# Kernel tuning notes

Measured on AMD Instinct MI355X. Metric: run time of the kernel, lower is better.

Reference implementation:

```python
import jax, jax.numpy as jnp
import numpy as np

B, P, D = 256, 128, 768        # batch, property slots per sample, encoder hidden dim
E = 64                          # num_properties (number of adapter heads)
H = 256                         # adapter_hidden_dim
H2 = H // 2
O = 2                           # output_dim
LN_EPS = 1e-5
RES_W_ADPT, RES_W_BASE = 0.7, 0.3


def setup_inputs() -> dict:
    key = jax.random.key(0)
    ks = jax.random.split(key, 12)
    hidden_states = jax.random.normal(ks[0], (B, P, D), dtype=jnp.float32)
    base_output = jax.random.normal(ks[1], (B, P, O), dtype=jnp.float32)
    properties = jax.random.randint(ks[2], (B, P), 0, E, dtype=jnp.int64)
    mask = (jax.random.uniform(ks[3], (B, P)) > 0.1).astype(jnp.float32)
    # Stacked per-head adapter parameters (LayerNorm + 3 Linears per head)
    ln_g = jnp.ones((E, D), dtype=jnp.float32)
    ln_b = jnp.zeros((E, D), dtype=jnp.float32)
    W1 = jax.random.normal(ks[4], (E, D, H), dtype=jnp.float32) * (1.0 / np.sqrt(D))
    b1 = jnp.zeros((E, H), dtype=jnp.float32)
    W2 = jax.random.normal(ks[5], (E, H, H2), dtype=jnp.float32) * (1.0 / np.sqrt(H))
    b2 = jnp.zeros((E, H2), dtype=jnp.float32)
    W3 = jax.random.normal(ks[6], (E, H2, O), dtype=jnp.float32) * 0.01  # init std=0.01 per source
    b3 = jnp.zeros((E, O), dtype=jnp.float32)
    return {
        "hidden_states": hidden_states, "base_output": base_output,
        "properties": properties, "mask": mask,
        "ln_g": ln_g, "ln_b": ln_b, "W1": W1, "b1": b1,
        "W2": W2, "b2": b2, "W3": W3, "b3": b3,
    }


def reference(hidden_states, base_output, properties, mask,
              ln_g, ln_b, W1, b1, W2, b2, W3, b3):
    b, p, d = hidden_states.shape
    o = W3.shape[-1]
    x = hidden_states.reshape(-1, d)                        # [N, D]
    # LayerNorm statistics are head-independent; only gamma/beta differ per head
    mu = jnp.mean(x, axis=-1, keepdims=True)
    var = jnp.mean((x - mu) ** 2, axis=-1, keepdims=True)
    xhat = (x - mu) * jax.lax.rsqrt(var + LN_EPS)           # [N, D]
    flat_p = properties.reshape(-1)                         # [N]
    flat_m = mask.reshape(-1)                               # [N]

    def body(acc, inp):
        idx, g, bt, w1, bb1, w2, bb2, w3, bb3 = inp
        h = jax.nn.relu((xhat * g + bt) @ w1 + bb1)         # [N, H]  (dropout = identity in eval)
        h = jax.nn.relu(h @ w2 + bb2)                       # [N, H2]
        out = h @ w3 + bb3                                  # [N, O]
        sel = (flat_p == idx) & (flat_m > 0)
        return jnp.where(sel[:, None], out, acc), None

    e = W1.shape[0]
    acc0 = jnp.zeros((b * p, o), dtype=x.dtype)
    acc, _ = jax.lax.scan(
        body, acc0,
        (jnp.arange(e), ln_g, ln_b, W1, b1, W2, b2, W3, b3))
    out = acc.reshape(b, p, o)
    out = RES_W_ADPT * out + RES_W_BASE * base_output       # use_residual=True
    return out * mask[..., None]
```

## Files before the change

kernel.cpp:

```cpp
#include <hip/hip_runtime.h>
#include <stdint.h>

typedef unsigned short u16;
typedef unsigned int   u32;

#define NTOK   32768
#define GD     768
#define GH     256
#define GH2    128
#define GE     64

typedef __bf16 bf16x8 __attribute__((ext_vector_type(8)));
typedef float  f32x4  __attribute__((ext_vector_type(4)));
union Frag { uint4 u; bf16x8 b; };

__device__ __forceinline__ float bf2f(u16 h) {
  union { u32 u; float f; } v; v.u = ((u32)h) << 16; return v.f;
}
__device__ __forceinline__ u16 f2bf(float f) {
  union { float f; u32 u; } v; v.f = f;
  u32 r = (v.u + 0x7fffu + ((v.u >> 16) & 1u)) >> 16;
  return (u16)r;
}

__device__ __forceinline__ void async16(void* lds, const void* g) {
  __builtin_amdgcn_global_load_lds(
      (const __attribute__((address_space(1))) void*)g,
      (__attribute__((address_space(3))) void*)lds, 16, 0, 0);
}

__device__ __forceinline__ int getProp(const int* p32, int t, int is64) {
  return is64 ? p32[2 * t] : p32[t];
}

static const size_t OFF_W1T  = 0;
static const size_t OFF_W2T  = 25165824;
static const size_t OFF_TOK  = 29360128;
static const size_t OFF_META = 29491200;

__global__ void setup_kernel(const int* __restrict__ prop, const float* __restrict__ mask,
                             u32* __restrict__ outz, int* __restrict__ counts2d,
                             int* __restrict__ cursors_p, int* __restrict__ flagp) {
  __shared__ int h[GE];
  __shared__ int vOr;
  const int b = blockIdx.x;
  const int tid = threadIdx.x;
  outz[b * 512 + tid] = 0u;
  outz[b * 512 + 256 + tid] = 0u;
  if (b < 4) cursors_p[b * 256 + tid] = 0;
  if (tid < GE) h[tid] = 0;
  if (tid == 0) vOr = 0;
  __syncthreads();
  int v = prop[2 * tid + 1] | prop[2 * (tid + 256) + 1];
  if (v) atomicOr(&vOr, 1);
  __syncthreads();
  const int is64 = (vOr == 0) ? 1 : 0;
  if (b == 0 && tid == 0) *flagp = is64;
  const int t = b * 256 + tid;
  if (mask[t] > 0.f) atomicAdd(&h[getProp(prop, t, is64)], 1);
  __syncthreads();
  if (tid < GE) counts2d[b * GE + tid] = h[tid];
}

__global__ void transpose_w1(const float* __restrict__ in, u16* __restrict__ out) {
  __shared__ u16 tl[64][260];
  const int bid = blockIdx.x;
  const int e  = bid / 12, r = bid % 12;
  const int d0 = (r / 4) * 256, h0 = (r % 4) * 64;
  const int tid = threadIdx.x;
  const size_t inMat = (size_t)e * GD * GH;
  const size_t outMat = (size_t)e * GH * GD;
  const int h_l = (tid & 15) * 4, d_l = tid >> 4;
#pragma unroll
  for (int dd = 0; dd < 16; ++dd) {
    const int d = d_l + dd * 16;
    float4 v = *(const float4*)(in + inMat + (size_t)(d0 + d) * GH + h0 + h_l);
    tl[h_l + 0][d] = f2bf(v.x);
    tl[h_l + 1][d] = f2bf(v.y);
    tl[h_l + 2][d] = f2bf(v.z);
    tl[h_l + 3][d] = f2bf(v.w);
  }
  __syncthreads();
  const int wv = tid >> 6, ln = tid & 63;
#pragma unroll
  for (int hh = 0; hh < 16; ++hh) {
    const int h = wv * 16 + hh;
    *(uint2*)(out + outMat + (size_t)(h0 + h) * GD + d0 + ln * 4) =
        *(const uint2*)&tl[h][ln * 4];
  }
}

__global__ void transpose_kernel(const float* __restrict__ in, u16* __restrict__ out,
                                 int R, int C, int tilesC) {
  __shared__ u16 tile[32][33];
  const int tilesPerMat = (R >> 5) * tilesC;
  const int e  = blockIdx.x / tilesPerMat;
  const int t  = blockIdx.x % tilesPerMat;
  const int tr = t / tilesC, tc = t % tilesC;
  const size_t mat = (size_t)e * R * C;
  const int tx = threadIdx.x & 31, ty = threadIdx.x >> 5;
  const int r0 = tr * 32, c0 = tc * 32;
#pragma unroll
  for (int i = 0; i < 32; i += 8)
    tile[ty + i][tx] = f2bf(in[mat + (size_t)(r0 + ty + i) * C + c0 + tx]);
  __syncthreads();
#pragma unroll
  for (int i = 0; i < 32; i += 8)
    out[mat + (size_t)(c0 + ty + i) * R + r0 + tx] = tile[tx][ty + i];
}

__global__ void scan_kernel(const int* __restrict__ counts2d, int* __restrict__ offsets,
                            int* __restrict__ tileHead, int* __restrict__ tileRow,
                            int* __restrict__ nTilesPtr) {
  __shared__ int part[4][GE];
  const int tid = threadIdx.x;
  const int e = tid & 63, q = tid >> 6;
  int c = 0;
  for (int b = q * 32; b < q * 32 + 32; ++b) c += counts2d[b * GE + e];
  part[q][e] = c;
  __syncthreads();
  if (tid < GE) {
    const int ct = part[0][e] + part[1][e] + part[2][e] + part[3][e];
    int inc = ct;
#pragma unroll
    for (int d = 1; d < 64; d <<= 1) { int n = __shfl_up(inc, d); if (e >= d) inc += n; }
    const int off = inc - ct;
    offsets[e] = off;
    if (e == 63) offsets[64] = inc;
    int ntile = (ct + 63) >> 6;
    int inct = ntile;
#pragma unroll
    for (int d = 1; d < 64; d <<= 1) { int n = __shfl_up(inct, d); if (e >= d) inct += n; }
    const int tb = inct - ntile;
    for (int j = 0; j < ntile; ++j) { tileHead[tb + j] = e; tileRow[tb + j] = off + j * 64; }
    if (e == 63) *nTilesPtr = inct;
  }
}

__global__ void scatter_kernel(const int* __restrict__ prop, const float* __restrict__ mask,
                               const int* __restrict__ offsets, int* __restrict__ cursors_p,
                               int* __restrict__ tokenIds, const int* __restrict__ flag) {
  __shared__ int h[GE];
  __shared__ int basebin[GE];
  const int tid = threadIdx.x;
  const int t = blockIdx.x * 256 + tid;
  if (tid < GE) h[tid] = 0;
  __syncthreads();
  int p = -1, rank = 0;
  if (mask[t] > 0.f) {
    p = getProp(prop, t, *flag);
    rank = atomicAdd(&h[p], 1);
  }
  __syncthreads();
  if (tid < GE && h[tid] > 0) basebin[tid] = atomicAdd(&cursors_p[tid * 16], h[tid]);
  __syncthreads();
  if (p >= 0) tokenIds[offsets[p] + basebin[p] + rank] = t;
}

__global__ __launch_bounds__(256, 2) void adapter_gemm(
    const float* __restrict__ hs, const u16* __restrict__ w1t, const u16* __restrict__ w2t,
    const float* __restrict__ lng, const float* __restrict__ lnb,
    const float* __restrict__ b1, const float* __restrict__ b2,
    const float* __restrict__ w3, const float* __restrict__ b3,
    const float* __restrict__ base, const float* __restrict__ mask,
    const int* __restrict__ tokenIds, const int* __restrict__ offsets,
    const int* __restrict__ tileHead, const int* __restrict__ tileRow,
    const int* __restrict__ nTilesPtr, float* __restrict__ outp) {
  __shared__ union LU {
    struct { u16 A[2][2048]; u16 B[2][8192]; } s;
    u16 h[17408];
  } uni;
  __shared__ u16 sB2[2][4096];
  __shared__ float sBias1[256];
  __shared__ float sBias2[128];
  __shared__ float sW3[2][128];
  __shared__ float sB3[2];
  __shared__ int   sTok[64];
  __shared__ __align__(16) float sGam[GD];
  __shared__ __align__(16) float sBet[GD];
  __shared__ float sMu[64];
  __shared__ float sRstd[64];

  const int tid  = threadIdx.x;
  const int wv   = tid >> 6;
  const int ln   = tid & 63;
  const int l15  = tid & 15;
  const int quad = (tid & 63) >> 4;
  const f32x4 vzero = {0.f, 0.f, 0.f, 0.f};
  const int nt = *nTilesPtr;

  for (int tile = blockIdx.x; tile < nt; tile += gridDim.x) {
    __syncthreads();
    const int e  = tileHead[tile];
    const int rs = tileRow[tile];
    const int nRows = min(64, offsets[e + 1] - rs);

    if (tid < 64) sTok[tid] = tokenIds[rs + min(tid, nRows - 1)];
    sBias1[tid] = b1[e * GH + tid];
    if (tid < 128) sBias2[tid] = b2[e * GH2 + tid];
    { const int k = tid >> 1, o = tid & 1; sW3[o][k] = w3[e * GH2 * 2 + k * 2 + o]; }
    if (tid < 2) sB3[tid] = b3[e * 2 + tid];
    __syncthreads();

    const u16* w1e = w1t + (size_t)e * GH * GD;
    const u16* w2e = w2t + (size_t)e * GH2 * GH;

#pragma unroll
    for (int j = 0; j < 4; ++j)
      async16(uni.s.B[0] + wv * 2048 + j * 512,
              w1e + (size_t)(j * 64 + ln) * GD + wv * 8);

    if (tid < 192) {
      *(float4*)&sGam[tid * 4] = *(const float4*)(lng + (size_t)e * GD + tid * 4);
      *(float4*)&sBet[tid * 4] = *(const float4*)(lnb + (size_t)e * GD + tid * 4);
    }

#pragma unroll 2
    for (int pass = 0; pass < 4; ++pass) {
      const int row = pass * 16 + (tid >> 4);
      const int l16 = tid & 15;
      const float* xp = hs + (size_t)sTok[row] * GD + l16 * 4;
      float s = 0.f, sq = 0.f;
#pragma unroll
      for (int c = 0; c < 12; ++c) {
        float4 u = *(const float4*)(xp + c * 64);
        s  += u.x + u.y + u.z + u.w;
        sq += u.x*u.x + u.y*u.y + u.z*u.z + u.w*u.w;
      }
#pragma unroll
      for (int d = 1; d < 16; d <<= 1) { s += __shfl_xor(s, d); sq += __shfl_xor(sq, d); }
      if (l16 == 0) {
        const float mu = s * (1.f / 768.f);
        sMu[row] = mu;
        sRstd[row] = rsqrtf(sq * (1.f / 768.f) - mu * mu + 1e-5f);
      }
    }
    __syncthreads();

    const int r0  = tid >> 3;
    const int klo = (tid & 7) * 4;
    const int kgrp = klo >> 3, kin = klo & 7;
    const float* xA = hs + (size_t)sTok[r0] * GD + klo;
    const float* xB = hs + (size_t)sTok[r0 + 32] * GD + klo;
    const float muA = sMu[r0],      rsA = sRstd[r0];
    const float muB = sMu[r0 + 32], rsB = sRstd[r0 + 32];

#define STAGE_A(K0, PAR) do {                                                   \
    const float4 gv = *(const float4*)&sGam[(K0) + klo];                        \
    const float4 bv = *(const float4*)&sBet[(K0) + klo];                        \
    float4 va = *(const float4*)(xA + (K0));                                    \
    float4 vb = *(const float4*)(xB + (K0));                                    \
    uint2 oa, ob;                                                               \
    oa.x = (u32)f2bf((va.x - muA) * rsA * gv.x + bv.x)                          \
         | ((u32)f2bf((va.y - muA) * rsA * gv.y + bv.y) << 16);                 \
    oa.y = (u32)f2bf((va.z - muA) * rsA * gv.z + bv.z)                          \
         | ((u32)f2bf((va.w - muA) * rsA * gv.w + bv.w) << 16);                 \
    ob.x = (u32)f2bf((vb.x - muB) * rsB * gv.x + bv.x)                          \
         | ((u32)f2bf((vb.y - muB) * rsB * gv.y + bv.y) << 16);                 \
    ob.y = (u32)f2bf((vb.z - muB) * rsB * gv.z + bv.z)                          \
         | ((u32)f2bf((vb.w - muB) * rsB * gv.w + bv.w) << 16);                 \
    *(uint2*)&uni.s.A[PAR][kgrp * 512 + r0 * 8 + kin] = oa;                     \
    *(uint2*)&uni.s.A[PAR][kgrp * 512 + (r0 + 32) * 8 + kin] = ob;              \
  } while (0)

    f32x4 acc1[4][4];
#pragma unroll
    for (int f = 0; f < 4; ++f)
#pragma unroll
      for (int g = 0; g < 4; ++g) acc1[f][g] = vzero;

    STAGE_A(0, 0);

    for (int kt = 0; kt < 24; ++kt) {
      __syncthreads();
      if (kt + 1 < 24) {
        const int k0 = (kt + 1) * 32;
        const int par = (kt + 1) & 1;
#pragma unroll
        for (int j = 0; j < 4; ++j)
          async16(uni.s.B[par] + wv * 2048 + j * 512,
                  w1e + (size_t)(j * 64 + ln) * GD + k0 + wv * 8);
        STAGE_A(k0, par);
      }
      const int par = kt & 1;
      Frag fa[4], fb[4];
#pragma unroll
      for (int f = 0; f < 4; ++f)
        fa[f].u = *(const uint4*)&uni.s.A[par][quad * 512 + (f * 16 + l15) * 8];
#pragma unroll
      for (int g = 0; g < 4; ++g)
        fb[g].u = *(const uint4*)&uni.s.B[par][quad * 2048 + (wv * 64 + g * 16 + l15) * 8];
#pragma unroll
      for (int f = 0; f < 4; ++f)
#pragma unroll
        for (int g = 0; g < 4; ++g)
          acc1[f][g] = __builtin_amdgcn_mfma_f32_16x16x32_bf16(fa[f].b, fb[g].b, acc1[f][g], 0, 0, 0);
    }
    __syncthreads();

#pragma unroll
    for (int j = 0; j < 2; ++j)
      async16(sB2[0] + wv * 1024 + j * 512,
              w2e + (size_t)(j * 64 + ln) * GH + wv * 8);

#pragma unroll
    for (int f = 0; f < 4; ++f)
#pragma unroll
      for (int g = 0; g < 4; ++g) {
        const int col = wv * 64 + g * 16 + l15;
        const float bias = sBias1[col];
#pragma unroll
        for (int r = 0; r < 4; ++r) {
          const int row = f * 16 + quad * 4 + r;
          uni.h[row * 264 + col] = f2bf(fmaxf(acc1[f][g][r] + bias, 0.f));
        }
      }

    f32x4 acc2[4][2];
#pragma unroll
    for (int f = 0; f < 4; ++f)
#pragma unroll
      for (int g = 0; g < 2; ++g) acc2[f][g] = vzero;

    for (int kt = 0; kt < 8; ++kt) {
      __syncthreads();
      if (kt + 1 < 8) {
        const int k0 = (kt + 1) * 32;
        const int par = (kt + 1) & 1;
#pragma unroll
        for (int j = 0; j < 2; ++j)
          async16(sB2[par] + wv * 1024 + j * 512,
                  w2e + (size_t)(j * 64 + ln) * GH + k0 + wv * 8);
      }
      const int par = kt & 1;
      Frag fa2[4], fb2[2];
#pragma unroll
      for (int f = 0; f < 4; ++f)
        fa2[f].u = *(const uint4*)&uni.h[(f * 16 + l15) * 264 + kt * 32 + quad * 8];
#pragma unroll
      for (int g = 0; g < 2; ++g)
        fb2[g].u = *(const uint4*)&sB2[par][quad * 1024 + (wv * 32 + g * 16 + l15) * 8];
#pragma unroll
      for (int f = 0; f < 4; ++f)
#pragma unroll
        for (int g = 0; g < 2; ++g)
          acc2[f][g] = __builtin_amdgcn_mfma_f32_16x16x32_bf16(fa2[f].b, fb2[g].b, acc2[f][g], 0, 0, 0);
    }
    __syncthreads();

#pragma unroll
    for (int f = 0; f < 4; ++f)
#pragma unroll
      for (int g = 0; g < 2; ++g) {
        const int col = wv * 32 + g * 16 + l15;
        const float bias = sBias2[col];
#pragma unroll
        for (int r = 0; r < 4; ++r) {
          const int row = f * 16 + quad * 4 + r;
          uni.h[row * 130 + col] = f2bf(fmaxf(acc2[f][g][r] + bias, 0.f));
        }
      }
    __syncthreads();

    const int m = tid >> 1, o = tid & 1;
    if (m < nRows) {
      float a = sB3[o];
      const u16* h2row = &uni.h[m * 130];
#pragma unroll 16
      for (int k = 0; k < 128; ++k) a += bf2f(h2row[k]) * sW3[o][k];
      const int t = sTok[m];
      const float mk = mask[t];
      const float bs = base[t * 2 + o];
      outp[t * 2 + o] = (0.7f * a + 0.3f * bs) * mk;
    }
  }
#undef STAGE_A
}

extern "C" void kernel_launch(void* const* d_in, const int* in_sizes, int n_in,
                              void* d_out, int out_size, void* d_ws, size_t ws_size,
                              hipStream_t stream) {
  const float* hs   = (const float*)d_in[0];
  const float* base = (const float*)d_in[1];
  const int*   prop = (const int*)d_in[2];
  const float* mask = (const float*)d_in[3];
  const float* lng  = (const float*)d_in[4];
  const float* lnb  = (const float*)d_in[5];
  const float* W1   = (const float*)d_in[6];
  const float* b1   = (const float*)d_in[7];
  const float* W2   = (const float*)d_in[8];
  const float* b2   = (const float*)d_in[9];
  const float* W3   = (const float*)d_in[10];
  const float* b3   = (const float*)d_in[11];

  char* ws = (char*)d_ws;
  u16* w1t  = (u16*)(ws + OFF_W1T);
  u16* w2t  = (u16*)(ws + OFF_W2T);
  int* tok  = (int*)(ws + OFF_TOK);
  int* meta = (int*)(ws + OFF_META);
  int* counts2d  = meta;
  int* offsets   = meta + 8192;
  int* tileHead  = meta + 8320;
  int* tileRow   = meta + 9344;
  int* nTiles    = meta + 10368;
  int* propFlag  = meta + 10369;
  int* cursors_p = meta + 10432;

  setup_kernel<<<128, 256, 0, stream>>>(prop, mask, (u32*)d_out, counts2d,
                                        cursors_p, propFlag);
  transpose_w1<<<768, 256, 0, stream>>>(W1, w1t);
  transpose_kernel<<<64 * 8 * 4, 256, 0, stream>>>(W2, w2t, GH, GH2, 4);
  scan_kernel<<<1, 256, 0, stream>>>(counts2d, offsets, tileHead, tileRow, nTiles);
  scatter_kernel<<<NTOK / 256, 256, 0, stream>>>(prop, mask, offsets, cursors_p, tok, propFlag);
  adapter_gemm<<<640, 256, 0, stream>>>(hs, w1t, w2t, lng, lnb, b1, b2, W3, b3,
                                        base, mask, tok, offsets, tileHead, tileRow,
                                        nTiles, (float*)d_out);
}
```

Baseline: 276.6 us.

## Pre-tile transposed weights to LDS fragment order and remap tile-to-block assignment

The W1 and W2 transpose kernels now write bf16 weights directly in the blocked layout the GEMM's LDS staging uses. Each async 16-byte load in the k-loop then reads one contiguous chunk instead of strided rows. The persistent GEMM loop also remaps its iteration index so that consecutive blocks take tiles spread across eight contiguous segments, which changes which heads run together and how weights are reused in L2. This adds a more complex tiled layout and index math, and the new tile order may affect cache locality.

```diff
diff --git a/kernel.cpp b/kernel.cpp
--- a/kernel.cpp
+++ b/kernel.cpp
@@ -82,31 +82,35 @@
   }
   __syncthreads();
   const int wv = tid >> 6, ln = tid & 63;
+  const int d_glob = d0 + ln * 4;
+  const size_t tbase = outMat + (size_t)(d_glob >> 5) * 8192 +
+                       (size_t)((d_glob >> 3) & 3) * 2048 + (d_glob & 7);
 #pragma unroll
   for (int hh = 0; hh < 16; ++hh) {
     const int h = wv * 16 + hh;
-    *(uint2*)(out + outMat + (size_t)(h0 + h) * GD + d0 + ln * 4) =
-        *(const uint2*)&tl[h][ln * 4];
+    *(uint2*)(out + tbase + (size_t)(h0 + h) * 8) = *(const uint2*)&tl[h][ln * 4];
   }
 }
 
-__global__ void transpose_kernel(const float* __restrict__ in, u16* __restrict__ out,
-                                 int R, int C, int tilesC) {
+__global__ void transpose_w2(const float* __restrict__ in, u16* __restrict__ out) {
   __shared__ u16 tile[32][33];
-  const int tilesPerMat = (R >> 5) * tilesC;
+  const int tilesPerMat = 32;
   const int e  = blockIdx.x / tilesPerMat;
   const int t  = blockIdx.x % tilesPerMat;
-  const int tr = t / tilesC, tc = t % tilesC;
-  const size_t mat = (size_t)e * R * C;
+  const int tr = t / 4, tc = t % 4;
+  const size_t mat = (size_t)e * GH * GH2;
   const int tx = threadIdx.x & 31, ty = threadIdx.x >> 5;
   const int r0 = tr * 32, c0 = tc * 32;
 #pragma unroll
   for (int i = 0; i < 32; i += 8)
-    tile[ty + i][tx] = f2bf(in[mat + (size_t)(r0 + ty + i) * C + c0 + tx]);
-  __syncthreads();
+    tile[ty + i][tx] = f2bf(in[mat + (size_t)(r0 + ty + i) * GH2 + c0 + tx]);
+  __syncthreads();
+  const int k = r0 + tx;
+  const size_t kbase = mat + (size_t)(k >> 5) * 4096 +
+                       (size_t)((k >> 3) & 3) * 1024 + (k & 7);
 #pragma unroll
   for (int i = 0; i < 32; i += 8)
-    out[mat + (size_t)(c0 + ty + i) * R + r0 + tx] = tile[tx][ty + i];
+    out[kbase + (size_t)(c0 + ty + i) * 8] = tile[tx][ty + i];
 }
 
 __global__ void scan_kernel(const int* __restrict__ counts2d, int* __restrict__ offsets,
@@ -188,8 +192,12 @@
   const int quad = (tid & 63) >> 4;
   const f32x4 vzero = {0.f, 0.f, 0.f, 0.f};
   const int nt = *nTilesPtr;
-
-  for (int tile = blockIdx.x; tile < nt; tile += gridDim.x) {
+  const int qq = nt >> 3, rr = nt & 7;
+
+  for (int i = blockIdx.x; i < nt; i += gridDim.x) {
+    const int x = i & 7, s = i >> 3;
+    const int tile = (x < rr ? x * (qq + 1) : rr * (qq + 1) + (x - rr) * qq) + s;
+
     __syncthreads();
     const int e  = tileHead[tile];
     const int rs = tileRow[tile];
@@ -208,7 +216,7 @@
 #pragma unroll
     for (int j = 0; j < 4; ++j)
       async16(uni.s.B[0] + wv * 2048 + j * 512,
-              w1e + (size_t)(j * 64 + ln) * GD + wv * 8);
+              w1e + wv * 2048 + j * 512 + ln * 8);
 
     if (tid < 192) {
       *(float4*)&sGam[tid * 4] = *(const float4*)(lng + (size_t)e * GD + tid * 4);
@@ -220,17 +228,17 @@
       const int row = pass * 16 + (tid >> 4);
       const int l16 = tid & 15;
       const float* xp = hs + (size_t)sTok[row] * GD + l16 * 4;
-      float s = 0.f, sq = 0.f;
+      float sm = 0.f, sq = 0.f;
 #pragma unroll
       for (int c = 0; c < 12; ++c) {
         float4 u = *(const float4*)(xp + c * 64);
-        s  += u.x + u.y + u.z + u.w;
+        sm += u.x + u.y + u.z + u.w;
         sq += u.x*u.x + u.y*u.y + u.z*u.z + u.w*u.w;
       }
 #pragma unroll
-      for (int d = 1; d < 16; d <<= 1) { s += __shfl_xor(s, d); sq += __shfl_xor(sq, d); }
+      for (int d = 1; d < 16; d <<= 1) { sm += __shfl_xor(sm, d); sq += __shfl_xor(sq, d); }
       if (l16 == 0) {
-        const float mu = s * (1.f / 768.f);
+        const float mu = sm * (1.f / 768.f);
         sMu[row] = mu;
         sRstd[row] = rsqrtf(sq * (1.f / 768.f) - mu * mu + 1e-5f);
       }
@@ -274,13 +282,12 @@
     for (int kt = 0; kt < 24; ++kt) {
       __syncthreads();
       if (kt + 1 < 24) {
-        const int k0 = (kt + 1) * 32;
         const int par = (kt + 1) & 1;
 #pragma unroll
         for (int j = 0; j < 4; ++j)
           async16(uni.s.B[par] + wv * 2048 + j * 512,
-                  w1e + (size_t)(j * 64 + ln) * GD + k0 + wv * 8);
-        STAGE_A(k0, par);
+                  w1e + (kt + 1) * 8192 + wv * 2048 + j * 512 + ln * 8);
+        STAGE_A((kt + 1) * 32, par);
       }
       const int par = kt & 1;
       Frag fa[4], fb[4];
@@ -301,7 +308,7 @@
 #pragma unroll
     for (int j = 0; j < 2; ++j)
       async16(sB2[0] + wv * 1024 + j * 512,
-              w2e + (size_t)(j * 64 + ln) * GH + wv * 8);
+              w2e + wv * 1024 + j * 512 + ln * 8);
 
 #pragma unroll
     for (int f = 0; f < 4; ++f)
@@ -325,12 +332,11 @@
     for (int kt = 0; kt < 8; ++kt) {
       __syncthreads();
       if (kt + 1 < 8) {
-        const int k0 = (kt + 1) * 32;
         const int par = (kt + 1) & 1;
 #pragma unroll
         for (int j = 0; j < 2; ++j)
           async16(sB2[par] + wv * 1024 + j * 512,
-                  w2e + (size_t)(j * 64 + ln) * GH + k0 + wv * 8);
+                  w2e + (kt + 1) * 4096 + wv * 1024 + j * 512 + ln * 8);
       }
       const int par = kt & 1;
       Frag fa2[4], fb2[2];
@@ -409,7 +415,7 @@
   setup_kernel<<<128, 256, 0, stream>>>(prop, mask, (u32*)d_out, counts2d,
                                         cursors_p, propFlag);
   transpose_w1<<<768, 256, 0, stream>>>(W1, w1t);
-  transpose_kernel<<<64 * 8 * 4, 256, 0, stream>>>(W2, w2t, GH, GH2, 4);
+  transpose_w2<<<64 * 32, 256, 0, stream>>>(W2, w2t);
   scan_kernel<<<1, 256, 0, stream>>>(counts2d, offsets, tileHead, tileRow, nTiles);
   scatter_kernel<<<NTOK / 256, 256, 0, stream>>>(prop, mask, offsets, cursors_p, tok, propFlag);
   adapter_gemm<<<640, 256, 0, stream>>>(hs, w1t, w2t, lng, lnb, b1, b2, W3, b3,
```

Result: faster. 260.7 us (-5.8%).
